# Kernel tuning notes

Measured on AMD Instinct MI355X. Metric: run time of the kernel, lower is better.

The kernel has to match this reference:

```python
import jax, jax.numpy as jnp
import numpy as np

B, N, C = 4, 262144, 10
K_PRE, K_POST = 4096, 500          # before_nms_max, after_nms_max
ROI_THR, NMS_THR = 0.1, 0.01       # roi_threshold, nms_threshold


def setup_inputs() -> dict:
    key = jax.random.key(0)
    k1, k2, k3, k4 = jax.random.split(key, 4)
    # raw logits; sigmoid(-2 + noise) straddles roi_threshold=0.1 realistically
    cls = jax.random.normal(k1, (B, N, C), jnp.float32) - 2.0
    centers = jax.random.uniform(k2, (B, N, 3), jnp.float32, minval=-50.0, maxval=50.0)
    sizes = jax.random.uniform(k3, (B, N, 3), jnp.float32, minval=0.5, maxval=5.0)
    heading = jax.random.uniform(k4, (B, N, 1), jnp.float32, minval=-np.pi, maxval=np.pi)
    boxes = jnp.concatenate([centers, sizes, heading], axis=-1)  # (B, N, 7)
    return {"batch_cls_preds": cls, "batch_box_preds": boxes}


def _pairwise_bev_iou(b):
    # b: (K, 7) = [x, y, z, dx, dy, dz, heading]; BEV IoU (heading ignored,
    # axis-aligned approximation of the rotated-IoU CUDA kernel).
    x, y, dx, dy = b[:, 0], b[:, 1], b[:, 3], b[:, 4]
    x1, x2 = x - dx * 0.5, x + dx * 0.5
    y1, y2 = y - dy * 0.5, y + dy * 0.5
    ix = jnp.clip(jnp.minimum(x2[:, None], x2[None, :]) - jnp.maximum(x1[:, None], x1[None, :]), 0.0)
    iy = jnp.clip(jnp.minimum(y2[:, None], y2[None, :]) - jnp.maximum(y1[:, None], y1[None, :]), 0.0)
    inter = ix * iy                              # (K, K)
    area = dx * dy                               # (K,)
    union = area[:, None] + area[None, :] - inter
    return inter / jnp.maximum(union, 1e-6)


def _nms_one(scores, labels, boxes):
    # scores: (N,), labels: (N,) int32, boxes: (N, 7)
    s = jnp.where(scores > ROI_THR, scores, -1.0)       # score-threshold filter
    topv, topi = jax.lax.top_k(s, K_PRE)                # keep top before_nms_max
    tb = boxes[topi]                                     # (K_PRE, 7)
    tl = labels[topi]
    iou = _pairwise_bev_iou(tb)                          # (K_PRE, K_PRE)
    keep0 = topv > ROI_THR

    def body(i, keep):
        # a kept higher-score box i suppresses later boxes with IoU > thr
        sup = (iou[i] > NMS_THR) & (jnp.arange(K_PRE) > i) & keep[i]
        return keep & ~sup

    keep = jax.lax.fori_loop(0, K_PRE, body, keep0)
    kept_scores = jnp.where(keep, topv, -1.0)
    fv, fi = jax.lax.top_k(kept_scores, K_POST)          # after_nms_max slots
    m = fv > 0.0
    final_scores = jnp.where(m, fv, 0.0)                 # (K_POST,)
    final_boxes = tb[fi] * m[:, None].astype(tb.dtype)   # (K_POST, 7)
    final_labels = jnp.where(m, tl[fi], -1)              # (K_POST,)
    return final_scores, final_boxes, final_labels


def reference(batch_cls_preds, batch_box_preds):
    probs = jax.nn.sigmoid(batch_cls_preds)              # (B, N, C)
    scores = jnp.max(probs, axis=-1)                     # per-anchor best class score
    labels = jnp.argmax(probs, axis=-1).astype(jnp.int32)
    final_scores, final_boxes, final_labels = jax.vmap(_nms_one)(scores, labels, batch_box_preds)
    return final_scores, final_boxes, final_labels
```

## Files before the change

### kernel.cpp

```cpp
#include <hip/hip_runtime.h>
#include <stdint.h>

constexpr int B = 4;
constexpr int N = 262144;
constexpr int C = 10;
constexpr int KPRE = 4096;
constexpr int KPOST = 500;
constexpr float ROI_THR = 0.1f;
constexpr float NMS_THR = 0.01f;
constexpr int CAP = 8192;
constexpr int MASKW = KPRE / 64;
constexpr int RJT = 2;
constexpr int MAXP = 32;

__device__ __forceinline__ uint32_t f2k(float f) {
  uint32_t u = __float_as_uint(f);
  return (u & 0x80000000u) ? ~u : (u | 0x80000000u);
}
__device__ __forceinline__ float k2f(uint32_t k) {
  uint32_t u = (k & 0x80000000u) ? (k ^ 0x80000000u) : ~k;
  return __uint_as_float(u);
}
__device__ __forceinline__ float sigm(float x) { return 1.0f / (1.0f + expf(-x)); }

__device__ __forceinline__ void async_lds16(const void* g, void* l) {
  __builtin_amdgcn_global_load_lds((const __attribute__((address_space(1))) void*)g,
                                   (__attribute__((address_space(3))) void*)l, 16, 0, 0);
}

__device__ __forceinline__ uint2 select256(const uint32_t* __restrict__ h, uint32_t R,
                                           uint32_t* s, uint32_t* o2) {
  int t = threadIdx.x;
  s[t] = h[t];
  __syncthreads();
  for (int off = 1; off < 256; off <<= 1) {
    uint32_t v = s[t] + ((t + off < 256) ? s[t + off] : 0u);
    __syncthreads();
    s[t] = v;
    __syncthreads();
  }
  uint32_t suf = s[t];
  uint32_t sufn = (t < 255) ? s[t + 1] : 0u;
  if (suf >= R && R > sufn) {
    o2[0] = (uint32_t)t;
    o2[1] = R - sufn;
  }
  __syncthreads();
  uint2 r;
  r.x = o2[0];
  r.y = o2[1];
  __syncthreads();
  return r;
}

__global__ void zeroK(uint32_t* __restrict__ p, int n) {
  int i = blockIdx.x * 256 + threadIdx.x;
  if (i < n) p[i] = 0u;
}

__global__ void scoreK(const float* __restrict__ cls, uint32_t* __restrict__ keys,
                       uint32_t* __restrict__ hist0) {
  __shared__ float ls[2560];
  __shared__ uint32_t h[256];
  int b = blockIdx.y;
  int t = threadIdx.x;
  h[t] = 0;
  size_t base = ((size_t)b * N + (size_t)blockIdx.x * 256) * C;
  const float2* g2 = (const float2*)(cls + base);
  float2* l2 = (float2*)ls;
#pragma unroll
  for (int r = 0; r < 5; ++r) l2[r * 256 + t] = g2[r * 256 + t];
  __syncthreads();
  const float* mine = ls + t * 10;
  float m = mine[0];
#pragma unroll
  for (int c = 1; c < C; ++c) m = fmaxf(m, mine[c]);
  float p = sigm(m);
  float sc = (p > ROI_THR) ? p : -1.0f;
  uint32_t k = f2k(sc);
  keys[(size_t)b * N + blockIdx.x * 256 + t] = k;
  atomicAdd(&h[k >> 24], 1u);
  __syncthreads();
  if (h[t]) atomicAdd(&hist0[b * 256 + t], h[t]);
}

__global__ void histP1K(const uint32_t* __restrict__ keys, const uint32_t* __restrict__ hist0,
                        uint32_t* __restrict__ hist1) {
  __shared__ uint32_t s[256];
  __shared__ uint32_t o2[2];
  __shared__ uint32_t h[256];
  int b = blockIdx.y;
  int t = threadIdx.x;
  uint2 s0 = select256(hist0 + b * 256, (uint32_t)KPRE, s, o2);
  h[t] = 0;
  __syncthreads();
  uint32_t pref = s0.x;
  const uint4* kb4 = (const uint4*)(keys + (size_t)b * N);
#pragma unroll
  for (int r = 0; r < 2; ++r) {
    uint4 kv = kb4[blockIdx.x * 512 + r * 256 + t];
#pragma unroll
    for (int j = 0; j < 4; ++j) {
      uint32_t k = (&kv.x)[j];
      if ((k >> 24) == pref) atomicAdd(&h[(k >> 16) & 255u], 1u);
    }
  }
  __syncthreads();
  if (h[t]) atomicAdd(&hist1[b * 256 + t], h[t]);
}

__global__ void compactK(const uint32_t* __restrict__ keys, const uint32_t* __restrict__ hist0,
                         const uint32_t* __restrict__ hist1, unsigned long long* __restrict__ list,
                         uint32_t* __restrict__ cnt) {
  __shared__ uint32_t s[256];
  __shared__ uint32_t o2[2];
  __shared__ uint32_t scan[256];
  __shared__ uint32_t baseSh;
  int b = blockIdx.y;
  int t = threadIdx.x;
  uint2 s0 = select256(hist0 + b * 256, (uint32_t)KPRE, s, o2);
  uint2 s1 = select256(hist1 + b * 256, s0.y, s, o2);
  uint32_t T = ((s0.x << 8) | s1.x) << 16;
  const uint4* kb4 = (const uint4*)(keys + (size_t)b * N);
  uint4 kv[4];
#pragma unroll
  for (int r = 0; r < 4; ++r) kv[r] = kb4[blockIdx.x * 1024 + r * 256 + t];
  uint32_t c = 0;
#pragma unroll
  for (int r = 0; r < 4; ++r)
#pragma unroll
    for (int j = 0; j < 4; ++j) c += ((&kv[r].x)[j] >= T) ? 1u : 0u;
  scan[t] = c;
  __syncthreads();
  for (int off = 1; off < 256; off <<= 1) {
    uint32_t v = scan[t] + ((t >= off) ? scan[t - off] : 0u);
    __syncthreads();
    scan[t] = v;
    __syncthreads();
  }
  uint32_t excl = scan[t] - c;
  if (t == 255) baseSh = atomicAdd(&cnt[b], scan[255]);
  __syncthreads();
  uint32_t pos = baseSh + excl;
#pragma unroll
  for (int r = 0; r < 4; ++r)
#pragma unroll
    for (int j = 0; j < 4; ++j) {
      uint32_t k = (&kv[r].x)[j];
      if (k >= T) {
        uint32_t n = (blockIdx.x * 1024 + r * 256 + t) * 4 + j;
        if (pos < CAP)
          list[(size_t)b * CAP + pos] = ((unsigned long long)k << 32) | (uint32_t)(~n);
        pos++;
      }
    }
}

__global__ void rankK(const unsigned long long* __restrict__ list, const uint32_t* __restrict__ cnt,
                      uint32_t* __restrict__ rank) {
  __shared__ unsigned long long lp[256];
  int b = blockIdx.z;
  int cc = (int)min(cnt[b], (uint32_t)CAP);
  if (blockIdx.x * 256 >= cc) return;
  int j0 = blockIdx.y * (256 * RJT);
  if (j0 >= cc) return;
  int i = blockIdx.x * 256 + threadIdx.x;
  unsigned long long pi = (i < cc) ? list[(size_t)b * CAP + i] : ~0ull;
  uint32_t c = 0;
#pragma unroll
  for (int tb = 0; tb < RJT; ++tb) {
    int j = j0 + tb * 256 + threadIdx.x;
    __syncthreads();
    lp[threadIdx.x] = (j < cc) ? list[(size_t)b * CAP + j] : 0ull;
    __syncthreads();
#pragma unroll 8
    for (int jj = 0; jj < 256; ++jj) c += (lp[jj] > pi) ? 1u : 0u;
  }
  if (i < cc && c) atomicAdd(&rank[(size_t)b * CAP + i], c);
}

__global__ void scatterK(const unsigned long long* __restrict__ list,
                         const uint32_t* __restrict__ cnt, const uint32_t* __restrict__ rank,
                         const float* __restrict__ boxes, float* __restrict__ sel_score,
                         uint32_t* __restrict__ sel_idx, float* __restrict__ sel_box) {
  int b = blockIdx.y;
  int p = blockIdx.x * 256 + threadIdx.x;
  uint32_t cc = min(cnt[b], (uint32_t)CAP);
  if (p >= (int)cc) return;
  unsigned long long pk = list[(size_t)b * CAP + p];
  uint32_t r = rank[(size_t)b * CAP + p];
  if (r >= (uint32_t)KPRE) return;
  uint32_t key = (uint32_t)(pk >> 32);
  uint32_t idx = ~(uint32_t)pk;
  sel_score[b * KPRE + r] = k2f(key);
  sel_idx[b * KPRE + r] = idx;
  const float* src = boxes + ((size_t)b * N + idx) * 7;
  float* dst = sel_box + ((size_t)b * KPRE + r) * 8;
#pragma unroll
  for (int c = 0; c < 7; ++c) dst[c] = src[c];
  dst[7] = 0.f;
}

template <bool CHK>
__device__ __forceinline__ void mask_row64(int tt, const float4* __restrict__ jv,
                                           const float* __restrict__ ja, float x1i, float x2i,
                                           float y1i, float y2i, float ai, uint32_t& lo0,
                                           uint32_t& hi0, uint32_t& band) {
#pragma unroll 16
  for (int jj = 0; jj < 64; ++jj) {
    float4 v = jv[jj];
    float aj = ja[jj];
    float xx1 = fmaxf(x1i, v.x), xx2 = fminf(x2i, v.y);
    float yy1 = fmaxf(y1i, v.z), yy2 = fminf(y2i, v.w);
    float ix = fmaxf(__fsub_rn(xx2, xx1), 0.0f), iy = fmaxf(__fsub_rn(yy2, yy1), 0.0f);
    float inter = __fmul_rn(ix, iy);
    float den = fmaxf(__fsub_rn(__fadd_rn(ai, aj), inter), 1e-6f);
    float q0 = __fmul_rn(NMS_THR, den);
    float d = __fsub_rn(inter, q0);
    band |= (fabsf(d) <= __fmul_rn(q0, 1e-5f)) ? 1u : 0u;
    bool sup = d > 0.0f;
    if (CHK) sup = sup && (jj > tt);
    uint32_t bit = sup ? 1u : 0u;
    if (jj < 32) lo0 |= bit << jj; else hi0 |= bit << (jj - 32);
  }
}

__global__ __launch_bounds__(64) void maskK(const float* __restrict__ sel_box,
                                            unsigned long long* __restrict__ maskT,
                                            unsigned long long* __restrict__ Tmat) {
  int b = blockIdx.z;
  int bi = blockIdx.x;
  int w = blockIdx.y;
  if (w < bi) return;
  int t = threadIdx.x;
  int i = bi * 64 + t;
  int j0 = w * 64;
  __shared__ float4 jv[64];
  __shared__ float ja[64];
  {
    const float4* bj = (const float4*)(sel_box + ((size_t)b * KPRE + j0 + t) * 8);
    float4 lo = bj[0], hi = bj[1];
    float xj = lo.x, yj = lo.y, dxj = lo.w, dyj = hi.x;
    float hxj = __fmul_rn(dxj, 0.5f), hyj = __fmul_rn(dyj, 0.5f);
    float4 v;
    v.x = __fsub_rn(xj, hxj);
    v.y = __fadd_rn(xj, hxj);
    v.z = __fsub_rn(yj, hyj);
    v.w = __fadd_rn(yj, hyj);
    jv[t] = v;
    ja[t] = __fmul_rn(dxj, dyj);
  }
  __syncthreads();
  const float4* myb = (const float4*)(sel_box + ((size_t)b * KPRE + i) * 8);
  float4 lo = myb[0], hi = myb[1];
  float x = lo.x, y = lo.y, dx = lo.w, dy = hi.x;
  float hx = __fmul_rn(dx, 0.5f), hy = __fmul_rn(dy, 0.5f);
  float x1i = __fsub_rn(x, hx), x2i = __fadd_rn(x, hx);
  float y1i = __fsub_rn(y, hy), y2i = __fadd_rn(y, hy);
  float ai = __fmul_rn(dx, dy);
  uint32_t lo0 = 0, hi0 = 0, band = 0;
  if (w == bi)
    mask_row64<true>(t, jv, ja, x1i, x2i, y1i, y2i, ai, lo0, hi0, band);
  else
    mask_row64<false>(t, jv, ja, x1i, x2i, y1i, y2i, ai, lo0, hi0, band);
  if (__builtin_expect(__any(band != 0), 0)) {
    lo0 = hi0 = 0;
    for (int jj = 0; jj < 64; ++jj) {
      float4 v = jv[jj];
      float aj = ja[jj];
      float xx1 = fmaxf(x1i, v.x), xx2 = fminf(x2i, v.y);
      float yy1 = fmaxf(y1i, v.z), yy2 = fminf(y2i, v.w);
      float ix = fmaxf(__fsub_rn(xx2, xx1), 0.0f), iy = fmaxf(__fsub_rn(yy2, yy1), 0.0f);
      float inter = __fmul_rn(ix, iy);
      float den = fmaxf(__fsub_rn(__fadd_rn(ai, aj), inter), 1e-6f);
      bool sup = (inter / den) > NMS_THR && (j0 + jj > i);
      uint32_t bit = sup ? 1u : 0u;
      if (jj < 32) lo0 |= bit << jj; else hi0 |= bit << (jj - 32);
    }
  }
  unsigned long long wacc = ((unsigned long long)hi0 << 32) | lo0;
  maskT[((size_t)b * MASKW + w) * KPRE + i] = wacc;
  if (w == bi) {
    unsigned long long m = wacc;
    unsigned long long T = 0ull;
#pragma unroll
    for (int j = 0; j < 64; ++j) {
      unsigned long long bj = __ballot(((m >> j) & 1ull) != 0ull);
      if (t == j) T = bj;
    }
    unsigned long long* trow = Tmat + ((size_t)b * 64 + w) * 128;
    trow[t] = T;
    trow[64 + t] = m;
  }
}

__global__ void nmsK(const unsigned long long* __restrict__ maskT,
                     const unsigned long long* __restrict__ Tmat,
                     const float* __restrict__ sel_score,
                     uint32_t* __restrict__ kept_pos, uint32_t* __restrict__ kept_cnt) {
  __shared__ unsigned long long td[64][128];
  __shared__ uint32_t keptbuf[KPOST];
  int b = blockIdx.x;
  int t = threadIdx.x;

  const char* tsrc = (const char*)(Tmat + (size_t)b * 64 * 128);
  for (int g = 0; g < 64; ++g)
    async_lds16(tsrc + (size_t)g * 1024 + (size_t)t * 16, &td[g][0]);

  unsigned long long cand = 0ull;
  for (int k = 0; k < 64; ++k) {
    float s = sel_score[b * KPRE + k * 64 + t];
    unsigned long long bal = __ballot(s > ROI_THR);
    if (t == k) cand = bal;
  }
  asm volatile("s_waitcnt vmcnt(0)" ::: "memory");

  const unsigned long long* mbt = maskT + (size_t)b * KPRE * MASKW + (size_t)t * KPRE;
  unsigned long long remv = 0ull;
  unsigned long long r[MAXP];
#pragma unroll
  for (int a = 0; a < MAXP; ++a) r[a] = 0ull;
  int kc = 0;

  for (int g = 0; g < 64; ++g) {
#pragma unroll
    for (int a = 0; a < MAXP; ++a) remv |= r[a];

    unsigned long long cw = cand & ~remv;
    unsigned long long aw =
        ((unsigned long long)(uint32_t)__builtin_amdgcn_readlane((uint32_t)(cw >> 32), g) << 32) |
        (uint32_t)__builtin_amdgcn_readlane((uint32_t)cw, g);
    if (aw) {
      unsigned long long T = td[g][t];
      unsigned long long m = td[g][64 + t];
      unsigned long long K = __ballot((m & aw) != 0ull);
      unsigned long long alive = aw;
      unsigned long long rem = aw & K;
      if (rem) {
        bool deadf = ((aw >> t) & 1ull) == 0ull;
        while (rem) {
          int s = __ffsll((long long)rem) - 1;
          rem &= rem - 1ull;
          if ((alive >> s) & 1ull) {
            deadf = deadf || (((T >> s) & 1ull) != 0ull);
            alive = __ballot(!deadf);
            rem &= alive;
          }
        }
      }
      int grp = __popcll(alive);
      if ((alive >> t) & 1ull) {
        int rk = __popcll(alive & ((1ull << t) - 1ull));
        if (kc + rk < KPOST) keptbuf[kc + rk] = (uint32_t)(g * 64 + t);
      }
      kc += grp;
      unsigned long long a2 = alive;
      bool again = true;
      while (again) {
#pragma unroll
        for (int a = 0; a < MAXP; ++a) {
          if (a2) {
            int s2 = __ffsll((long long)a2) - 1;
            a2 &= a2 - 1ull;
            r[a] = (t >= g) ? mbt[g * 64 + s2] : 0ull;
          } else {
            r[a] = 0ull;
          }
        }
        if (a2) {
#pragma unroll
          for (int a = 0; a < MAXP; ++a) {
            remv |= r[a];
            r[a] = 0ull;
          }
          again = true;
        } else {
          again = false;
        }
      }
      if (kc >= KPOST) break;
    } else {
#pragma unroll
      for (int a = 0; a < MAXP; ++a) r[a] = 0ull;
    }
  }
  asm volatile("s_waitcnt vmcnt(0)" ::: "memory");
  int kcc = min(kc, KPOST);
  for (int i = t; i < kcc; i += 64) kept_pos[b * KPOST + i] = keptbuf[i];
  if (t == 0) kept_cnt[b] = (uint32_t)kcc;
}

__global__ void outK(const float* __restrict__ cls,
                     const float* __restrict__ sel_score, const uint32_t* __restrict__ sel_idx,
                     const float* __restrict__ sel_box,
                     const uint32_t* __restrict__ kept_pos, const uint32_t* __restrict__ kept_cnt,
                     float* __restrict__ out) {
  int b = blockIdx.y;
  int s = blockIdx.x * blockDim.x + threadIdx.x;
  if (s >= KPOST) return;
  float* oS = out;
  float* oB = out + B * KPOST;
  float* oL = out + B * KPOST + B * KPOST * 7;
  uint32_t kcnt = kept_cnt[b];
  if (s < (int)kcnt) {
    uint32_t pos = kept_pos[b * KPOST + s];
    oS[b * KPOST + s] = sel_score[b * KPRE + pos];
    const float* box = sel_box + ((size_t)b * KPRE + pos) * 8;
    float* dst = oB + ((size_t)b * KPOST + s) * 7;
#pragma unroll
    for (int c = 0; c < 7; ++c) dst[c] = box[c];
    uint32_t idx = sel_idx[b * KPRE + pos];
    const float* p = cls + ((size_t)b * N + idx) * C;
    float bestv = sigm(p[0]);
    int bestc = 0;
#pragma unroll
    for (int c = 1; c < C; ++c) {
      float v = sigm(p[c]);
      if (v > bestv) { bestv = v; bestc = c; }
    }
    oL[b * KPOST + s] = (float)bestc;
  } else {
    oS[b * KPOST + s] = 0.0f;
    float* dst = oB + ((size_t)b * KPOST + s) * 7;
#pragma unroll
    for (int c = 0; c < 7; ++c) dst[c] = 0.0f;
    oL[b * KPOST + s] = -1.0f;
  }
}

__global__ void sentinelK(float* out, int n) {
  int i = blockIdx.x * blockDim.x + threadIdx.x;
  if (i < n) out[i] = 1337.0f;
}

extern "C" void kernel_launch(void* const* d_in, const int* in_sizes, int n_in,
                              void* d_out, int out_size, void* d_ws, size_t ws_size,
                              hipStream_t stream) {
  const float* cls = (const float*)d_in[0];
  const float* boxes = (const float*)d_in[1];
  float* out = (float*)d_out;

  char* ws = (char*)d_ws;
  size_t off = 0;
  auto alloc = [&](size_t bytes) -> void* {
    void* p = ws + off;
    off = (off + bytes + 255) & ~(size_t)255;
    return p;
  };
  size_t mask_bytes = (size_t)B * KPRE * MASKW * 8;
  unsigned long long* mask = (unsigned long long*)alloc(mask_bytes);
  unsigned long long* list = (unsigned long long*)alloc((size_t)B * CAP * 8);
  uint32_t* keys = (uint32_t*)alloc((size_t)B * N * 4);
  float* sel_box = (float*)alloc((size_t)B * KPRE * 8 * 4);
  float* sel_score = (float*)alloc((size_t)B * KPRE * 4);
  uint32_t* sel_idx = (uint32_t*)alloc((size_t)B * KPRE * 4);
  uint32_t* kept_pos = (uint32_t*)alloc((size_t)B * KPOST * 4);
  uint32_t* kept_cnt = (uint32_t*)alloc(B * 4);
  unsigned long long* Tmat = (unsigned long long*)alloc((size_t)B * 64 * 128 * 8);

  uint32_t* hist0 = (uint32_t*)mask;
  uint32_t* hist1 = hist0 + B * 256;
  uint32_t* cnt = hist1 + B * 256;
  uint32_t* rank = (uint32_t*)((char*)mask + 16384);
  int zwords = (16384 + B * CAP * 4) / 4;

  if (off > ws_size) {
    sentinelK<<<dim3((out_size + 255) / 256), 256, 0, stream>>>(out, out_size);
    return;
  }

  zeroK<<<dim3((zwords + 255) / 256), 256, 0, stream>>>((uint32_t*)mask, zwords);
  scoreK<<<dim3(N / 256, B), 256, 0, stream>>>(cls, keys, hist0);
  histP1K<<<dim3(N / 2048, B), 256, 0, stream>>>(keys, hist0, hist1);
  compactK<<<dim3(N / 4096, B), 256, 0, stream>>>(keys, hist0, hist1, list, cnt);
  rankK<<<dim3(CAP / 256, CAP / (256 * RJT), B), 256, 0, stream>>>(list, cnt, rank);
  scatterK<<<dim3(CAP / 256, B), 256, 0, stream>>>(list, cnt, rank, boxes, sel_score, sel_idx,
                                                   sel_box);
  maskK<<<dim3(64, 64, B), 64, 0, stream>>>(sel_box, mask, Tmat);
  nmsK<<<B, 64, 0, stream>>>(mask, Tmat, sel_score, kept_pos, kept_cnt);
  outK<<<dim3((KPOST + 255) / 256, B), 256, 0, stream>>>(cls, sel_score, sel_idx, sel_box,
                                                         kept_pos, kept_cnt, out);
}
```

Baseline: 140.0 us.

## Speculatively compact high-score candidates in scoreK to shrink later radix-select passes

scoreK now processes 1024 anchors per block. Alongside the keys it writes a compacted sublist of anchors whose sortable key is at or above the key for score 0.5. histP1K and compactK check whether the selected top radix byte is 0xBF and the sublist did not overflow. If so, they scan only the sublist instead of all N keys, cutting global memory traffic. Otherwise they fall back to the original full scans, at the cost of extra sublist writes and a block scan in scoreK.

```diff
diff --git a/kernel.cpp b/kernel.cpp
--- a/kernel.cpp
+++ b/kernel.cpp
@@ -12,6 +12,8 @@
 constexpr int MASKW = KPRE / 64;
 constexpr int RJT = 2;
 constexpr int MAXP = 32;
+constexpr int CAP05 = 131072;
+constexpr uint32_t SPEC_T = 0xBF000000u;
 
 __device__ __forceinline__ uint32_t f2k(float f) {
   uint32_t u = __float_as_uint(f);
@@ -59,33 +61,67 @@
 }
 
 __global__ void scoreK(const float* __restrict__ cls, uint32_t* __restrict__ keys,
-                       uint32_t* __restrict__ hist0) {
+                       uint32_t* __restrict__ hist0, unsigned long long* __restrict__ sublist,
+                       uint32_t* __restrict__ cnt05) {
   __shared__ float ls[2560];
   __shared__ uint32_t h[256];
+  __shared__ uint32_t scan[256];
+  __shared__ uint32_t baseSh;
   int b = blockIdx.y;
   int t = threadIdx.x;
   h[t] = 0;
-  size_t base = ((size_t)b * N + (size_t)blockIdx.x * 256) * C;
-  const float2* g2 = (const float2*)(cls + base);
-  float2* l2 = (float2*)ls;
-#pragma unroll
-  for (int r = 0; r < 5; ++r) l2[r * 256 + t] = g2[r * 256 + t];
-  __syncthreads();
-  const float* mine = ls + t * 10;
-  float m = mine[0];
-#pragma unroll
-  for (int c = 1; c < C; ++c) m = fmaxf(m, mine[c]);
-  float p = sigm(m);
-  float sc = (p > ROI_THR) ? p : -1.0f;
-  uint32_t k = f2k(sc);
-  keys[(size_t)b * N + blockIdx.x * 256 + t] = k;
-  atomicAdd(&h[k >> 24], 1u);
-  __syncthreads();
+  uint32_t kreg[4];
+#pragma unroll
+  for (int kk = 0; kk < 4; ++kk) {
+    int item0 = blockIdx.x * 1024 + kk * 256;
+    size_t base = ((size_t)b * N + item0) * C;
+    const float4* g4 = (const float4*)(cls + base);
+    float4* l4 = (float4*)ls;
+    __syncthreads();
+    for (int i = t; i < 640; i += 256) l4[i] = g4[i];
+    __syncthreads();
+    const float* mine = ls + t * 10;
+    float m = mine[0];
+#pragma unroll
+    for (int c = 1; c < C; ++c) m = fmaxf(m, mine[c]);
+    float p = sigm(m);
+    float sc = (p > ROI_THR) ? p : -1.0f;
+    uint32_t k = f2k(sc);
+    keys[(size_t)b * N + item0 + t] = k;
+    atomicAdd(&h[k >> 24], 1u);
+    kreg[kk] = k;
+  }
+  uint32_t cnt_t = 0;
+#pragma unroll
+  for (int kk = 0; kk < 4; ++kk) cnt_t += (kreg[kk] >= SPEC_T) ? 1u : 0u;
+  scan[t] = cnt_t;
+  __syncthreads();
+  for (int off = 1; off < 256; off <<= 1) {
+    uint32_t v = scan[t] + ((t >= off) ? scan[t - off] : 0u);
+    __syncthreads();
+    scan[t] = v;
+    __syncthreads();
+  }
+  uint32_t excl = scan[t] - cnt_t;
+  if (t == 255) baseSh = atomicAdd(&cnt05[b], scan[255]);
+  __syncthreads();
+  uint32_t pos = baseSh + excl;
+#pragma unroll
+  for (int kk = 0; kk < 4; ++kk) {
+    if (kreg[kk] >= SPEC_T) {
+      uint32_t n = (uint32_t)(blockIdx.x * 1024 + kk * 256 + t);
+      if (pos < (uint32_t)CAP05)
+        sublist[(size_t)b * CAP05 + pos] = ((unsigned long long)kreg[kk] << 32) | (uint32_t)(~n);
+      pos++;
+    }
+  }
   if (h[t]) atomicAdd(&hist0[b * 256 + t], h[t]);
 }
 
 __global__ void histP1K(const uint32_t* __restrict__ keys, const uint32_t* __restrict__ hist0,
-                        uint32_t* __restrict__ hist1) {
+                        uint32_t* __restrict__ hist1,
+                        const unsigned long long* __restrict__ sublist,
+                        const uint32_t* __restrict__ cnt05) {
   __shared__ uint32_t s[256];
   __shared__ uint32_t o2[2];
   __shared__ uint32_t h[256];
@@ -94,15 +130,25 @@
   uint2 s0 = select256(hist0 + b * 256, (uint32_t)KPRE, s, o2);
   h[t] = 0;
   __syncthreads();
-  uint32_t pref = s0.x;
-  const uint4* kb4 = (const uint4*)(keys + (size_t)b * N);
-#pragma unroll
-  for (int r = 0; r < 2; ++r) {
-    uint4 kv = kb4[blockIdx.x * 512 + r * 256 + t];
-#pragma unroll
-    for (int j = 0; j < 4; ++j) {
-      uint32_t k = (&kv.x)[j];
-      if ((k >> 24) == pref) atomicAdd(&h[(k >> 16) & 255u], 1u);
+  uint32_t c05 = cnt05[b];
+  bool fast = (s0.x == 0xBFu) && (c05 <= (uint32_t)CAP05);
+  if (fast) {
+    const unsigned long long* sl = sublist + (size_t)b * CAP05;
+    for (uint32_t i = blockIdx.x * 256 + t; i < c05; i += gridDim.x * 256) {
+      uint32_t k = (uint32_t)(sl[i] >> 32);
+      atomicAdd(&h[(k >> 16) & 255u], 1u);
+    }
+  } else {
+    uint32_t pref = s0.x;
+    const uint4* kb4 = (const uint4*)(keys + (size_t)b * N);
+#pragma unroll
+    for (int r = 0; r < 2; ++r) {
+      uint4 kv = kb4[blockIdx.x * 512 + r * 256 + t];
+#pragma unroll
+      for (int j = 0; j < 4; ++j) {
+        uint32_t k = (&kv.x)[j];
+        if ((k >> 24) == pref) atomicAdd(&h[(k >> 16) & 255u], 1u);
+      }
     }
   }
   __syncthreads();
@@ -110,8 +156,10 @@
 }
 
 __global__ void compactK(const uint32_t* __restrict__ keys, const uint32_t* __restrict__ hist0,
-                         const uint32_t* __restrict__ hist1, unsigned long long* __restrict__ list,
-                         uint32_t* __restrict__ cnt) {
+                         const uint32_t* __restrict__ hist1,
+                         const unsigned long long* __restrict__ sublist,
+                         const uint32_t* __restrict__ cnt05,
+                         unsigned long long* __restrict__ list, uint32_t* __restrict__ cnt) {
   __shared__ uint32_t s[256];
   __shared__ uint32_t o2[2];
   __shared__ uint32_t scan[256];
@@ -121,39 +169,65 @@
   uint2 s0 = select256(hist0 + b * 256, (uint32_t)KPRE, s, o2);
   uint2 s1 = select256(hist1 + b * 256, s0.y, s, o2);
   uint32_t T = ((s0.x << 8) | s1.x) << 16;
-  const uint4* kb4 = (const uint4*)(keys + (size_t)b * N);
-  uint4 kv[4];
-#pragma unroll
-  for (int r = 0; r < 4; ++r) kv[r] = kb4[blockIdx.x * 1024 + r * 256 + t];
-  uint32_t c = 0;
-#pragma unroll
-  for (int r = 0; r < 4; ++r)
-#pragma unroll
-    for (int j = 0; j < 4; ++j) c += ((&kv[r].x)[j] >= T) ? 1u : 0u;
-  scan[t] = c;
-  __syncthreads();
-  for (int off = 1; off < 256; off <<= 1) {
-    uint32_t v = scan[t] + ((t >= off) ? scan[t - off] : 0u);
-    __syncthreads();
-    scan[t] = v;
-    __syncthreads();
-  }
-  uint32_t excl = scan[t] - c;
-  if (t == 255) baseSh = atomicAdd(&cnt[b], scan[255]);
-  __syncthreads();
-  uint32_t pos = baseSh + excl;
-#pragma unroll
-  for (int r = 0; r < 4; ++r)
-#pragma unroll
-    for (int j = 0; j < 4; ++j) {
-      uint32_t k = (&kv[r].x)[j];
-      if (k >= T) {
-        uint32_t n = (blockIdx.x * 1024 + r * 256 + t) * 4 + j;
-        if (pos < CAP)
-          list[(size_t)b * CAP + pos] = ((unsigned long long)k << 32) | (uint32_t)(~n);
-        pos++;
-      }
-    }
+  uint32_t c05 = cnt05[b];
+  bool fast = (s0.x == 0xBFu) && (c05 <= (uint32_t)CAP05);
+  if (fast) {
+    const unsigned long long* sl = sublist + (size_t)b * CAP05;
+    for (uint32_t bi = blockIdx.x * 256; bi < c05; bi += gridDim.x * 256) {
+      uint32_t i = bi + t;
+      unsigned long long e = (i < c05) ? sl[i] : 0ull;
+      uint32_t fl = (i < c05 && (uint32_t)(e >> 32) >= T) ? 1u : 0u;
+      scan[t] = fl;
+      __syncthreads();
+      for (int off = 1; off < 256; off <<= 1) {
+        uint32_t v = scan[t] + ((t >= off) ? scan[t - off] : 0u);
+        __syncthreads();
+        scan[t] = v;
+        __syncthreads();
+      }
+      if (t == 255) baseSh = atomicAdd(&cnt[b], scan[255]);
+      __syncthreads();
+      if (fl) {
+        uint32_t pos = baseSh + scan[t] - 1;
+        if (pos < (uint32_t)CAP) list[(size_t)b * CAP + pos] = e;
+      }
+      __syncthreads();
+    }
+  } else {
+    const uint4* kb4 = (const uint4*)(keys + (size_t)b * N);
+    uint4 kv[4];
+#pragma unroll
+    for (int r = 0; r < 4; ++r) kv[r] = kb4[blockIdx.x * 1024 + r * 256 + t];
+    uint32_t c = 0;
+#pragma unroll
+    for (int r = 0; r < 4; ++r)
+#pragma unroll
+      for (int j = 0; j < 4; ++j) c += ((&kv[r].x)[j] >= T) ? 1u : 0u;
+    scan[t] = c;
+    __syncthreads();
+    for (int off = 1; off < 256; off <<= 1) {
+      uint32_t v = scan[t] + ((t >= off) ? scan[t - off] : 0u);
+      __syncthreads();
+      scan[t] = v;
+      __syncthreads();
+    }
+    uint32_t excl = scan[t] - c;
+    if (t == 255) baseSh = atomicAdd(&cnt[b], scan[255]);
+    __syncthreads();
+    uint32_t pos = baseSh + excl;
+#pragma unroll
+    for (int r = 0; r < 4; ++r)
+#pragma unroll
+      for (int j = 0; j < 4; ++j) {
+        uint32_t k = (&kv[r].x)[j];
+        if (k >= T) {
+          uint32_t n = (blockIdx.x * 1024 + r * 256 + t) * 4 + j;
+          if (pos < CAP)
+            list[(size_t)b * CAP + pos] = ((unsigned long long)k << 32) | (uint32_t)(~n);
+          pos++;
+        }
+      }
+  }
 }
 
 __global__ void rankK(const unsigned long long* __restrict__ list, const uint32_t* __restrict__ cnt,
@@ -457,10 +531,12 @@
   uint32_t* kept_pos = (uint32_t*)alloc((size_t)B * KPOST * 4);
   uint32_t* kept_cnt = (uint32_t*)alloc(B * 4);
   unsigned long long* Tmat = (unsigned long long*)alloc((size_t)B * 64 * 128 * 8);
+  unsigned long long* sublist = (unsigned long long*)alloc((size_t)B * CAP05 * 8);
 
   uint32_t* hist0 = (uint32_t*)mask;
   uint32_t* hist1 = hist0 + B * 256;
   uint32_t* cnt = hist1 + B * 256;
+  uint32_t* cnt05 = cnt + B;
   uint32_t* rank = (uint32_t*)((char*)mask + 16384);
   int zwords = (16384 + B * CAP * 4) / 4;
 
@@ -470,9 +546,9 @@
   }
 
   zeroK<<<dim3((zwords + 255) / 256), 256, 0, stream>>>((uint32_t*)mask, zwords);
-  scoreK<<<dim3(N / 256, B), 256, 0, stream>>>(cls, keys, hist0);
-  histP1K<<<dim3(N / 2048, B), 256, 0, stream>>>(keys, hist0, hist1);
-  compactK<<<dim3(N / 4096, B), 256, 0, stream>>>(keys, hist0, hist1, list, cnt);
+  scoreK<<<dim3(N / 1024, B), 256, 0, stream>>>(cls, keys, hist0, sublist, cnt05);
+  histP1K<<<dim3(N / 2048, B), 256, 0, stream>>>(keys, hist0, hist1, sublist, cnt05);
+  compactK<<<dim3(N / 4096, B), 256, 0, stream>>>(keys, hist0, hist1, sublist, cnt05, list, cnt);
   rankK<<<dim3(CAP / 256, CAP / (256 * RJT), B), 256, 0, stream>>>(list, cnt, rank);
   scatterK<<<dim3(CAP / 256, B), 256, 0, stream>>>(list, cnt, rank, boxes, sel_score, sel_idx,
                                                    sel_box);
```

New measurement: 145.5 us. +3.9%, slower.
